# Optimization experiments

Hardware: AMD Instinct MI355X
Metric: run time of the kernel (lower is better)

Reference implementation:

```python
import jax, jax.numpy as jnp
import numpy as np

N = 100000; D = 256; ATT = 512; H = 8; HD = ATT // H; E = 250000
TYPE_CT = 64; TS = 64; P = 8192; PC = 1024; MP = 131072; MC = 16384


def setup_inputs() -> dict:
    key = jax.random.key(0)
    ks = jax.random.split(key, 24)
    sD = 1.0 / np.sqrt(D); sT = 1.0 / np.sqrt(TS); sA = 1.0 / np.sqrt(ATT); sC = 1.0 / np.sqrt(D + ATT)
    inp = {}
    inp['node_states'] = jax.random.normal(ks[0], (N, D), jnp.float32)
    inp['node_types'] = jax.random.randint(ks[1], (N,), 0, TYPE_CT, jnp.int32)
    inp['pair_conj'] = jax.random.randint(ks[2], (E,), 0, N, jnp.int32)
    inp['pair_prem'] = jax.random.randint(ks[3], (E,), 0, N, jnp.int32)
    inp['pool_prem_nodes'] = jax.random.randint(ks[4], (MP,), 0, N, jnp.int32)
    inp['pool_prem_seg'] = ((jnp.arange(MP, dtype=jnp.int32) * P) // MP).astype(jnp.int32)  # every prem set non-empty
    inp['pool_conj_nodes'] = jax.random.randint(ks[5], (MC,), 0, N, jnp.int32)
    inp['pool_conj_seg'] = ((jnp.arange(MC, dtype=jnp.int32) * PC) // MC).astype(jnp.int32)
    inp['prem2conj'] = jax.random.randint(ks[6], (P,), 0, PC, jnp.int32)
    # learned parameters
    inp['ln_g'] = jnp.ones((D,), jnp.float32)
    inp['ln_b'] = jnp.zeros((D,), jnp.float32)
    inp['emb_p'] = jax.random.normal(ks[7], (TYPE_CT, TS), jnp.float32) * 0.02
    inp['wp_w'] = jax.random.normal(ks[8], (TS, ATT), jnp.float32) * sT
    inp['wp_b'] = jnp.zeros((ATT,), jnp.float32)
    inp['emb_c'] = jax.random.normal(ks[9], (TYPE_CT, TS), jnp.float32) * 0.02
    inp['wc_w'] = jax.random.normal(ks[10], (TS, ATT), jnp.float32) * sT
    inp['wc_b'] = jnp.zeros((ATT,), jnp.float32)
    inp['Wq_p'] = jax.random.normal(ks[11], (H, D, HD), jnp.float32) * sD
    inp['Wk_p'] = jax.random.normal(ks[12], (H, D, HD), jnp.float32) * sD
    inp['Wv_p'] = jax.random.normal(ks[13], (H, D, HD), jnp.float32) * sD
    inp['Wo_p'] = jax.random.normal(ks[14], (ATT, ATT), jnp.float32) * sA
    inp['Wq_c'] = jax.random.normal(ks[15], (H, D, HD), jnp.float32) * sD
    inp['Wk_c'] = jax.random.normal(ks[16], (H, D, HD), jnp.float32) * sD
    inp['Wv_c'] = jax.random.normal(ks[17], (H, D, HD), jnp.float32) * sD
    inp['Wo_c'] = jax.random.normal(ks[18], (ATT, ATT), jnp.float32) * sA
    inp['W_dag'] = jax.random.normal(ks[19], (D + ATT, D + ATT), jnp.float32) * sC
    inp['b_dag'] = jnp.zeros((D + ATT,), jnp.float32)
    return inp


def _layernorm(x, g, b):
    mu = jnp.mean(x, axis=-1, keepdims=True)
    var = jnp.mean(jnp.square(x - mu), axis=-1, keepdims=True)
    return (x - mu) * jax.lax.rsqrt(var + 1e-5) * g + b


def _mha_dir(x, src, tgt, Wq, Wk, Wv, Wo, gate):
    # gather query/key/value node reprs along the pair list (irregular gather)
    xs = x[src]; xt = x[tgt]                       # [E, D]
    q = jnp.einsum('ed,hdk->ehk', xs, Wq)          # [E, H, HD]
    k = jnp.einsum('ed,hdk->ehk', xt, Wk)
    scores = jnp.sum(q * k, axis=-1) / np.sqrt(HD)  # [E, H]
    # per-query-node (segment) softmax, as in compute_att_aggr grouping
    m = jax.ops.segment_max(scores, src, num_segments=N)
    ex = jnp.exp(scores - m[src])
    denom = jax.ops.segment_sum(ex, src, num_segments=N)
    prob = ex / denom[src]
    v = jnp.einsum('ed,hdk->ehk', xt, Wv)
    # adj_matr @ comb_matr scatter-aggregation
    agg = jax.ops.segment_sum(prob[..., None] * v, src, num_segments=N)  # [N, H, HD]
    return gate * (agg.reshape(N, H * HD) @ Wo)


def reference(node_states, node_types, pair_conj, pair_prem, pool_prem_nodes, pool_prem_seg,
              pool_conj_nodes, pool_conj_seg, prem2conj,
              ln_g, ln_b, emb_p, wp_w, wp_b, emb_c, wc_w, wc_b,
              Wq_p, Wk_p, Wv_p, Wo_p, Wq_c, Wk_c, Wv_c, Wo_c, W_dag, b_dag):
    x = _layernorm(node_states, ln_g, ln_b)                                  # ne_norm(node reprs)
    gate_p = jax.nn.sigmoid(emb_p[node_types] @ wp_w + wp_b)                 # prem_gate  [N, ATT]
    gate_c = jax.nn.sigmoid(emb_c[node_types] @ wc_w + wc_b)                 # conj_gate
    # just_prem pairs: (prem, conj) -> query/scatter node = prem, key/value node = conj
    comb = _mha_dir(x, pair_prem, pair_conj, Wq_p, Wk_p, Wv_p, Wo_p, gate_p)
    # just_conj pairs: (conj, prem)
    comb = comb + _mha_dir(x, pair_conj, pair_prem, Wq_c, Wk_c, Wv_c, Wo_c, gate_c)
    h = jnp.concatenate([x, comb], axis=1)                                   # [N, D+ATT]
    pooled = jnp.tanh(h @ W_dag + b_dag)                                     # simplified dag_lstm pass
    prem_r = jax.ops.segment_max(pooled[pool_prem_nodes], pool_prem_seg, num_segments=P)
    conj_sets = jax.ops.segment_max(pooled[pool_conj_nodes], pool_conj_seg, num_segments=PC)
    conj_r = conj_sets[prem2conj]
    return jnp.concatenate([prem_r, conj_r], axis=1)                         # [P, 2*(D+ATT)]
```

## Files before the change

### kernel.cpp

```cpp
#include <hip/hip_runtime.h>
#include <math.h>

#define N_NODES 100000
#define DIM 256
#define ATT 512
#define NH 8
#define HD 64
#define E_PAIRS 250000
#define TYPE_CT 64
#define TS 64
#define P_SEG 8192
#define PC_SEG 1024
#define MP_SZ 131072
#define MC_SZ 16384
#define CD 768

typedef unsigned short u16;
typedef __attribute__((ext_vector_type(8))) short short8v;
typedef __attribute__((ext_vector_type(4))) float floatx4;

__device__ __forceinline__ u16 f2b(float f) {
    unsigned u = __float_as_uint(f);
    return (u16)((u + 0x7FFFu + ((u >> 16) & 1u)) >> 16);
}
__device__ __forceinline__ float b2f(u16 h) {
    return __uint_as_float(((unsigned)h) << 16);
}

__global__ __launch_bounds__(256) void fill_val_k(float* out, int n, float v) {
    int i = blockIdx.x * 256 + threadIdx.x;
    if (i < n) out[i] = v;
}

__global__ __launch_bounds__(64) void layernorm_k(
    const float* __restrict__ ns, const float* __restrict__ g,
    const float* __restrict__ b, u16* __restrict__ x)
{
    int row = blockIdx.x;
    int lane = threadIdx.x;
    float4 v = ((const float4*)(ns + (size_t)row * DIM))[lane];
    float sum = v.x + v.y + v.z + v.w;
    #pragma unroll
    for (int off = 32; off >= 1; off >>= 1) sum += __shfl_xor(sum, off);
    float mu = sum * (1.0f / DIM);
    float dx = v.x - mu, dy = v.y - mu, dz = v.z - mu, dw = v.w - mu;
    float sq = dx * dx + dy * dy + dz * dz + dw * dw;
    #pragma unroll
    for (int off = 32; off >= 1; off >>= 1) sq += __shfl_xor(sq, off);
    float rs = rsqrtf(sq * (1.0f / DIM) + 1e-5f);
    float4 gg = ((const float4*)g)[lane];
    float4 bb = ((const float4*)b)[lane];
    u16 o4[4];
    o4[0] = f2b(dx * rs * gg.x + bb.x);
    o4[1] = f2b(dy * rs * gg.y + bb.y);
    o4[2] = f2b(dz * rs * gg.z + bb.z);
    o4[3] = f2b(dw * rs * gg.w + bb.w);
    *(uint2*)(x + (size_t)row * DIM + lane * 4) = *(uint2*)o4;
}

__global__ __launch_bounds__(512) void gate_table_k(
    const float* __restrict__ emb, const float* __restrict__ w,
    const float* __restrict__ wb, float* __restrict__ tab)
{
    int t = blockIdx.x;
    int a = threadIdx.x;
    float acc = wb[a];
    #pragma unroll 8
    for (int s = 0; s < TS; ++s) acc += emb[t * TS + s] * w[s * ATT + a];
    tab[t * ATT + a] = 1.0f / (1.0f + expf(-acc));
}

__global__ __launch_bounds__(256) void wcvt_k(
    const float* __restrict__ W, u16* __restrict__ Bt, int K, int N)
{
    int idx = blockIdx.x * 256 + threadIdx.x;
    if (idx >= K * N) return;
    int c = idx / K, k = idx - c * K;
    Bt[idx] = f2b(W[(size_t)k * N + c]);
}

__global__ __launch_bounds__(256) void wqkv_cvt_k(
    const float* __restrict__ Wq, const float* __restrict__ Wk,
    const float* __restrict__ Wv, u16* __restrict__ outp)
{
    int idx = blockIdx.x * 256 + threadIdx.x;
    if (idx >= NH * 3 * HD * DIM) return;
    int k = idx & (DIM - 1);
    int c = (idx >> 8) & (HD - 1);
    int hm = idx >> 14;
    int m = hm % 3;
    int h = hm / 3;
    const float* W = (m == 0) ? Wq : ((m == 1) ? Wk : Wv);
    outp[idx] = f2b(W[((size_t)h * DIM + k) * HD + c]);
}

template<int WN, int EPI>
__device__ __forceinline__ void gemm_body2(
    const u16* __restrict__ A, int lda,
    const u16* __restrict__ A2, int lda2, int K1,
    const u16* __restrict__ Bt, int ldb,
    u16* __restrict__ C, int ldc,
    int M, int K,
    const float* __restrict__ bias,
    const float* __restrict__ gateTab,
    const int* __restrict__ types)
{
    constexpr int BN = 32 * WN;
    constexpr int BR = BN / 64;
    __shared__ u16 As[2][128 * 32];
    __shared__ u16 Bs[2][BN * 32];
    const int bm = blockIdx.y * 128;
    const int bn = blockIdx.x * BN;
    const int tid = threadIdx.x;
    const int wave = tid >> 6, lane = tid & 63;
    const int wm = (wave >> 1) * 64, wn = (wave & 1) * 16 * WN;
    const int srow = tid >> 2;
    const int skk = (tid & 3) * 8;
    floatx4 acc[4][WN] = {};

    auto stage = [&](int buf, int k0) {
        #pragma unroll
        for (int rnd = 0; rnd < 2; ++rnd) {
            int grow = bm + srow + rnd * 64;
            if (grow > M - 1) grow = M - 1;
            int gk = k0 + skk;
            const u16* src;
            if (EPI == 2 && gk >= K1) src = A2 + (size_t)grow * lda2 + (gk - K1);
            else                      src = A + (size_t)grow * lda + gk;
            __builtin_amdgcn_global_load_lds(
                (const __attribute__((address_space(1))) void*)src,
                (__attribute__((address_space(3))) void*)(&As[buf][rnd * 2048 + wave * 512]),
                16, 0, 0);
        }
        #pragma unroll
        for (int rnd = 0; rnd < BR; ++rnd) {
            const u16* src = Bt + (size_t)(bn + srow + rnd * 64) * ldb + k0 + skk;
            __builtin_amdgcn_global_load_lds(
                (const __attribute__((address_space(1))) void*)src,
                (__attribute__((address_space(3))) void*)(&Bs[buf][rnd * 2048 + wave * 512]),
                16, 0, 0);
        }
    };

    stage(0, 0);
    int cur = 0;
    const int rr = lane & 15, kq = (lane >> 4) * 8;
    for (int k0 = 0; k0 < K; k0 += 32) {
        __syncthreads();
        if (k0 + 32 < K) stage(cur ^ 1, k0 + 32);
        short8v a[4], b[WN];
        #pragma unroll
        for (int i = 0; i < 4; ++i)
            a[i] = *(const short8v*)&As[cur][(wm + i * 16 + rr) * 32 + kq];
        #pragma unroll
        for (int j = 0; j < WN; ++j)
            b[j] = *(const short8v*)&Bs[cur][(wn + j * 16 + rr) * 32 + kq];
        #pragma unroll
        for (int i = 0; i < 4; ++i)
            #pragma unroll
            for (int j = 0; j < WN; ++j)
                acc[i][j] = __builtin_amdgcn_mfma_f32_16x16x32_bf16(
                    a[i], b[j], acc[i][j], 0, 0, 0);
        cur ^= 1;
    }
    #pragma unroll
    for (int i = 0; i < 4; ++i) {
        #pragma unroll
        for (int j = 0; j < WN; ++j) {
            #pragma unroll
            for (int q = 0; q < 4; ++q) {
                int row = bm + wm + i * 16 + (lane >> 4) * 4 + q;
                if (row >= M) continue;
                int col = bn + wn + j * 16 + (lane & 15);
                float v = acc[i][j][q];
                size_t idx = (size_t)row * ldc + col;
                if (EPI == 0) C[idx] = f2b(v);
                else if (EPI == 1) {
                    float g = gateTab[types[row] * ATT + col];
                    C[idx] = f2b(b2f(C[idx]) + g * v);
                } else if (EPI == 3) {
                    float g = gateTab[types[row] * ATT + col];
                    C[idx] = f2b(g * v);
                } else {
                    C[idx] = f2b(tanhf(v + bias[col]));
                }
            }
        }
    }
}

__global__ __launch_bounds__(256) void gemm_qkv(
    const u16* __restrict__ A, const u16* __restrict__ Bt, u16* __restrict__ C)
{
    gemm_body2<6, 0>(A, DIM, nullptr, 0, 1 << 30, Bt, DIM, C, 192,
                     N_NODES, DIM, nullptr, nullptr, nullptr);
}
__global__ __launch_bounds__(256) void gemm_wo_first(
    const u16* __restrict__ A, const u16* __restrict__ Bt, u16* __restrict__ C,
    const float* __restrict__ gateTab, const int* __restrict__ types)
{
    gemm_body2<4, 3>(A, ATT, nullptr, 0, 1 << 30, Bt, ATT, C, ATT,
                     N_NODES, ATT, nullptr, gateTab, types);
}
__global__ __launch_bounds__(256) void gemm_wo_acc(
    const u16* __restrict__ A, const u16* __restrict__ Bt, u16* __restrict__ C,
    const float* __restrict__ gateTab, const int* __restrict__ types)
{
    gemm_body2<4, 1>(A, ATT, nullptr, 0, 1 << 30, Bt, ATT, C, ATT,
                     N_NODES, ATT, nullptr, gateTab, types);
}
__global__ __launch_bounds__(256) void gemm_dag(
    const u16* __restrict__ A, const u16* __restrict__ A2,
    const u16* __restrict__ Bt, u16* __restrict__ C,
    const float* __restrict__ bias)
{
    gemm_body2<4, 2>(A, DIM, A2, ATT, DIM, Bt, CD, C, 384,
                     N_NODES, CD, bias, nullptr, nullptr);
}

__global__ __launch_bounds__(256) void count_k(
    const int* __restrict__ src, int* __restrict__ counts)
{
    int e = blockIdx.x * 256 + threadIdx.x;
    if (e < E_PAIRS) atomicAdd(&counts[src[e]], 1);
}
__global__ __launch_bounds__(256) void scan1_k(
    const int* __restrict__ counts, int* __restrict__ offs, int* __restrict__ bsums)
{
    __shared__ int sm[256];
    int i = blockIdx.x * 256 + threadIdx.x;
    int v = (i < N_NODES) ? counts[i] : 0;
    sm[threadIdx.x] = v;
    __syncthreads();
    for (int d = 1; d < 256; d <<= 1) {
        int t = (threadIdx.x >= d) ? sm[threadIdx.x - d] : 0;
        __syncthreads();
        sm[threadIdx.x] += t;
        __syncthreads();
    }
    if (i < N_NODES) offs[i] = sm[threadIdx.x] - v;
    if (threadIdx.x == 255) bsums[blockIdx.x] = sm[255];
}
__global__ __launch_bounds__(512) void scan2_k(int* __restrict__ bsums, int nb)
{
    __shared__ int sm[512];
    int tx = threadIdx.x;
    int v = (tx < nb) ? bsums[tx] : 0;
    sm[tx] = v;
    __syncthreads();
    for (int d = 1; d < 512; d <<= 1) {
        int t = (tx >= d) ? sm[tx - d] : 0;
        __syncthreads();
        sm[tx] += t;
        __syncthreads();
    }
    if (tx < nb) bsums[tx] = sm[tx] - v;
}
__global__ __launch_bounds__(256) void addcur_k(
    int* __restrict__ offs, const int* __restrict__ bsums, int* __restrict__ cur)
{
    int i = blockIdx.x * 256 + threadIdx.x;
    if (i >= N_NODES) return;
    int o = offs[i] + bsums[i >> 8];
    offs[i] = o;
    cur[i] = o;
}
__global__ __launch_bounds__(256) void scatter_k(
    const int* __restrict__ src, const int* __restrict__ tgt,
    int* __restrict__ cur, int* __restrict__ csr_tgt)
{
    int e = blockIdx.x * 256 + threadIdx.x;
    if (e >= E_PAIRS) return;
    int p = atomicAdd(&cur[src[e]], 1);
    csr_tgt[p] = tgt[e];
}

__global__ __launch_bounds__(256) void attn_k(
    const u16* __restrict__ qkv, const int* __restrict__ offs,
    const int* __restrict__ counts, const int* __restrict__ csr_tgt,
    u16* __restrict__ agg, int h)
{
    int s = blockIdx.x * 4 + (threadIdx.x >> 6);
    if (s >= N_NODES) return;
    int lane = threadIdx.x & 63;
    float q = b2f(qkv[(size_t)s * 192 + lane]) * 0.125f;
    int lo = offs[s], deg = counts[s];
    float m = -INFINITY, l = 0.0f, acc = 0.0f;
    for (int i = 0; i < deg; ++i) {
        int t = csr_tgt[lo + i];
        float kd = b2f(qkv[(size_t)t * 192 + 64 + lane]);
        float vd = b2f(qkv[(size_t)t * 192 + 128 + lane]);
        float p = q * kd;
        #pragma unroll
        for (int off = 32; off >= 1; off >>= 1) p += __shfl_xor(p, off);
        float mn = fmaxf(m, p);
        float sc = expf(m - mn);
        float w  = expf(p - mn);
        l = l * sc + w;
        acc = acc * sc + w * vd;
        m = mn;
    }
    float r = (deg > 0) ? acc / l : 0.0f;
    agg[(size_t)s * ATT + h * HD + lane] = f2b(r);
}

template<int BFOUT>
__global__ __launch_bounds__(256) void seg_max_k(
    const u16* __restrict__ pooled, const int* __restrict__ nodes,
    const int* __restrict__ seg, int total, void* __restrict__ outv, int ldo)
{
    int p = blockIdx.x;
    int lo, hi;
    { int a = 0, b2 = total; while (a < b2) { int mid = (a + b2) >> 1; if (seg[mid] < p) a = mid + 1; else b2 = mid; } lo = a; }
    { int a = lo, b2 = total; while (a < b2) { int mid = (a + b2) >> 1; if (seg[mid] < p + 1) a = mid + 1; else b2 = mid; } hi = a; }
    for (int c = threadIdx.x; c < 384; c += 256) {
        float mx = -INFINITY;
        for (int i = lo; i < hi; ++i)
            mx = fmaxf(mx, b2f(pooled[(size_t)nodes[i] * 384 + c]));
        if (BFOUT) ((u16*)outv)[(size_t)p * ldo + c] = f2b(mx);
        else       ((float*)outv)[(size_t)p * ldo + c] = mx;
    }
}

__global__ __launch_bounds__(768) void gather_conj(
    const u16* __restrict__ cs, const int* __restrict__ p2c,
    float* __restrict__ out)
{
    int p = blockIdx.x;
    int c = threadIdx.x;
    out[(size_t)p * (2 * CD) + CD + c] = b2f(cs[(size_t)p2c[p] * CD + c]);
}

extern "C" void kernel_launch(void* const* d_in, const int* in_sizes, int n_in,
                              void* d_out, int out_size, void* d_ws, size_t ws_size,
                              hipStream_t stream) {
    const float* node_states     = (const float*)d_in[0];
    const int*   node_types      = (const int*)d_in[1];
    const int*   pair_conj       = (const int*)d_in[2];
    const int*   pair_prem       = (const int*)d_in[3];
    const int*   pool_prem_nodes = (const int*)d_in[4];
    const int*   pool_prem_seg   = (const int*)d_in[5];
    const int*   pool_conj_nodes = (const int*)d_in[6];
    const int*   pool_conj_seg   = (const int*)d_in[7];
    const int*   prem2conj       = (const int*)d_in[8];
    const float* ln_g  = (const float*)d_in[9];
    const float* ln_b  = (const float*)d_in[10];
    const float* emb_p = (const float*)d_in[11];
    const float* wp_w  = (const float*)d_in[12];
    const float* wp_b  = (const float*)d_in[13];
    const float* emb_c = (const float*)d_in[14];
    const float* wc_w  = (const float*)d_in[15];
    const float* wc_b  = (const float*)d_in[16];
    const float* Wq_p  = (const float*)d_in[17];
    const float* Wk_p  = (const float*)d_in[18];
    const float* Wv_p  = (const float*)d_in[19];
    const float* Wo_p  = (const float*)d_in[20];
    const float* Wq_c  = (const float*)d_in[21];
    const float* Wk_c  = (const float*)d_in[22];
    const float* Wv_c  = (const float*)d_in[23];
    const float* Wo_c  = (const float*)d_in[24];
    const float* W_dag = (const float*)d_in[25];
    const float* b_dag = (const float*)d_in[26];
    float* out = (float*)d_out;

    char* ws = (char*)d_ws;
    size_t o = 0;
    u16* x_bf  = (u16*)(ws + o); o += (size_t)N_NODES * DIM * 2;
    u16* comb  = (u16*)(ws + o); o += (size_t)N_NODES * ATT * 2;
    u16* R     = (u16*)(ws + o); o += (size_t)N_NODES * ATT * 2;
    char* csrb = ws + o;         o += 8000000;
    u16* conj_sets = (u16*)(ws + o); o += (size_t)PC_SEG * CD * 2;
    const size_t WS_NEEDED = o;

    if (ws_size < WS_NEEDED) {
        fill_val_k<<<(out_size + 255) / 256, 256, 0, stream>>>(out, out_size, (float)ws_size);
        return;
    }

    u16* agg    = R;
    u16* pooled = R;
    int* c_counts[2], *c_offs[2], *c_cur[2], *c_tgt[2];
    for (int d = 0; d < 2; ++d) {
        char* base = csrb + (size_t)d * 2200000;
        c_counts[d] = (int*)(base + 0);
        c_offs[d]   = (int*)(base + 400000);
        c_cur[d]    = (int*)(base + 800000);
        c_tgt[d]    = (int*)(base + 1200000);
    }
    int* bsums = (int*)(csrb + 4400000);
    u16* wdag_t = (u16*)csrb;

    char* ob = (char*)d_out;
    u16* qkv     = (u16*)(ob + 0);
    float* gtab_p = (float*)(ob + 38400000);
    float* gtab_c = (float*)(ob + 38531072);
    u16* wqkv_t  = (u16*)(ob + 38662144);
    u16* wo_t    = (u16*)(ob + 40235008);

    layernorm_k<<<N_NODES, 64, 0, stream>>>(node_states, ln_g, ln_b, x_bf);
    gate_table_k<<<TYPE_CT, ATT, 0, stream>>>(emb_p, wp_w, wp_b, gtab_p);
    gate_table_k<<<TYPE_CT, ATT, 0, stream>>>(emb_c, wc_w, wc_b, gtab_c);
    wqkv_cvt_k<<<(NH * 3 * HD * DIM + 255) / 256, 256, 0, stream>>>(
        Wq_p, Wk_p, Wv_p, wqkv_t);
    wqkv_cvt_k<<<(NH * 3 * HD * DIM + 255) / 256, 256, 0, stream>>>(
        Wq_c, Wk_c, Wv_c, wqkv_t + (size_t)NH * 3 * HD * DIM);
    wcvt_k<<<(ATT * ATT + 255) / 256, 256, 0, stream>>>(Wo_p, wo_t, ATT, ATT);
    wcvt_k<<<(ATT * ATT + 255) / 256, 256, 0, stream>>>(
        Wo_c, wo_t + (size_t)ATT * ATT, ATT, ATT);

    const int NSCAN = (N_NODES + 255) / 256;
    for (int d = 0; d < 2; ++d) {
        const int* src = d ? pair_conj : pair_prem;
        const int* tgt = d ? pair_prem : pair_conj;
        hipMemsetAsync(c_counts[d], 0, 400000, stream);
        count_k<<<(E_PAIRS + 255) / 256, 256, 0, stream>>>(src, c_counts[d]);
        scan1_k<<<NSCAN, 256, 0, stream>>>(c_counts[d], c_offs[d], bsums);
        scan2_k<<<1, 512, 0, stream>>>(bsums, NSCAN);
        addcur_k<<<NSCAN, 256, 0, stream>>>(c_offs[d], bsums, c_cur[d]);
        scatter_k<<<(E_PAIRS + 255) / 256, 256, 0, stream>>>(src, tgt, c_cur[d], c_tgt[d]);
    }

    const int MB128 = (N_NODES + 127) / 128;

    for (int dir = 0; dir < 2; ++dir) {
        const float* gt = dir ? gtab_c : gtab_p;
        const u16* wq_d = wqkv_t + (size_t)dir * NH * 3 * HD * DIM;
        const u16* wo_d = wo_t + (size_t)dir * ATT * ATT;

        for (int h = 0; h < NH; ++h) {
            gemm_qkv<<<dim3(1, MB128), 256, 0, stream>>>(
                x_bf, wq_d + (size_t)h * 3 * HD * DIM, qkv);
            attn_k<<<(N_NODES + 3) / 4, 256, 0, stream>>>(
                qkv, c_offs[dir], c_counts[dir], c_tgt[dir], agg, h);
        }

        if (dir == 0)
            gemm_wo_first<<<dim3(ATT / 128, MB128), 256, 0, stream>>>(
                agg, wo_d, comb, gt, node_types);
        else
            gemm_wo_acc<<<dim3(ATT / 128, MB128), 256, 0, stream>>>(
                agg, wo_d, comb, gt, node_types);
    }

    wcvt_k<<<(CD * CD + 255) / 256, 256, 0, stream>>>(W_dag, wdag_t, CD, CD);

    for (int c0 = 0; c0 < CD; c0 += 384) {
        gemm_dag<<<dim3(3, MB128), 256, 0, stream>>>(
            x_bf, comb, wdag_t + (size_t)c0 * CD, pooled, b_dag + c0);
        seg_max_k<0><<<P_SEG, 256, 0, stream>>>(
            pooled, pool_prem_nodes, pool_prem_seg, MP_SZ, out + c0, 2 * CD);
        seg_max_k<1><<<PC_SEG, 256, 0, stream>>>(
            pooled, pool_conj_nodes, pool_conj_seg, MC_SZ, conj_sets + c0, CD);
    }
    gather_conj<<<P_SEG, CD, 0, stream>>>(conj_sets, prem2conj, out);
}
```

Baseline: 2.232 ms.

## Triple-buffer GEMM LDS staging with explicit vmcnt waits and raw barriers

Converts the shared bf16 GEMM body from double to triple buffering, so global-to-LDS loads are issued two k-steps ahead. Each iteration waits with an explicit s_waitcnt vmcnt on only the older outstanding loads and then issues a bare s_barrier, replacing __syncthreads. The goal is to hide global load latency behind MFMA work in all four projection GEMMs. The cost is 50% more LDS per block, which may lower occupancy, plus hand-counted waits that depend on how many loads each stage issues.

```diff
diff --git a/kernel.cpp b/kernel.cpp
--- a/kernel.cpp
+++ b/kernel.cpp
@@ -25,6 +25,15 @@
 }
 __device__ __forceinline__ float b2f(u16 h) {
     return __uint_as_float(((unsigned)h) << 16);
+}
+
+template<int N>
+__device__ __forceinline__ void waitcnt_vm() {
+    asm volatile("s_waitcnt vmcnt(%0)" :: "n"(N) : "memory");
+}
+__device__ __forceinline__ void barrier_fence() {
+    asm volatile("s_barrier" ::: "memory");
+    __builtin_amdgcn_sched_barrier(0);
 }
 
 __global__ __launch_bounds__(256) void fill_val_k(float* out, int n, float v) {
@@ -95,7 +104,7 @@
 }
 
 template<int WN, int EPI>
-__device__ __forceinline__ void gemm_body2(
+__device__ __forceinline__ void gemm_body3(
     const u16* __restrict__ A, int lda,
     const u16* __restrict__ A2, int lda2, int K1,
     const u16* __restrict__ Bt, int ldb,
@@ -107,8 +116,9 @@
 {
     constexpr int BN = 32 * WN;
     constexpr int BR = BN / 64;
-    __shared__ u16 As[2][128 * 32];
-    __shared__ u16 Bs[2][BN * 32];
+    constexpr int LA = 2 + BR;
+    __shared__ u16 As[3][128 * 32];
+    __shared__ u16 Bs[3][BN * 32];
     const int bm = blockIdx.y * 128;
     const int bn = blockIdx.x * BN;
     const int tid = threadIdx.x;
@@ -142,12 +152,16 @@
         }
     };
 
+    const int NS = K >> 5;
     stage(0, 0);
+    stage(1, 32);
+    const int rr = lane & 15, kq = (lane >> 4) * 8;
     int cur = 0;
-    const int rr = lane & 15, kq = (lane >> 4) * 8;
-    for (int k0 = 0; k0 < K; k0 += 32) {
-        __syncthreads();
-        if (k0 + 32 < K) stage(cur ^ 1, k0 + 32);
+    for (int is = 0; is < NS; ++is) {
+        if (is == NS - 1) waitcnt_vm<0>();
+        else              waitcnt_vm<LA>();
+        barrier_fence();
+        if (is + 2 < NS) stage((cur + 2) % 3, (is + 2) * 32);
         short8v a[4], b[WN];
         #pragma unroll
         for (int i = 0; i < 4; ++i)
@@ -161,7 +175,7 @@
             for (int j = 0; j < WN; ++j)
                 acc[i][j] = __builtin_amdgcn_mfma_f32_16x16x32_bf16(
                     a[i], b[j], acc[i][j], 0, 0, 0);
-        cur ^= 1;
+        cur = (cur + 1) % 3;
     }
     #pragma unroll
     for (int i = 0; i < 4; ++i) {
@@ -192,21 +206,21 @@
 __global__ __launch_bounds__(256) void gemm_qkv(
     const u16* __restrict__ A, const u16* __restrict__ Bt, u16* __restrict__ C)
 {
-    gemm_body2<6, 0>(A, DIM, nullptr, 0, 1 << 30, Bt, DIM, C, 192,
+    gemm_body3<6, 0>(A, DIM, nullptr, 0, 1 << 30, Bt, DIM, C, 192,
                      N_NODES, DIM, nullptr, nullptr, nullptr);
 }
 __global__ __launch_bounds__(256) void gemm_wo_first(
     const u16* __restrict__ A, const u16* __restrict__ Bt, u16* __restrict__ C,
     const float* __restrict__ gateTab, const int* __restrict__ types)
 {
-    gemm_body2<4, 3>(A, ATT, nullptr, 0, 1 << 30, Bt, ATT, C, ATT,
+    gemm_body3<4, 3>(A, ATT, nullptr, 0, 1 << 30, Bt, ATT, C, ATT,
                      N_NODES, ATT, nullptr, gateTab, types);
 }
 __global__ __launch_bounds__(256) void gemm_wo_acc(
     const u16* __restrict__ A, const u16* __restrict__ Bt, u16* __restrict__ C,
     const float* __restrict__ gateTab, const int* __restrict__ types)
 {
-    gemm_body2<4, 1>(A, ATT, nullptr, 0, 1 << 30, Bt, ATT, C, ATT,
+    gemm_body3<4, 1>(A, ATT, nullptr, 0, 1 << 30, Bt, ATT, C, ATT,
                      N_NODES, ATT, nullptr, gateTab, types);
 }
 __global__ __launch_bounds__(256) void gemm_dag(
@@ -214,7 +228,7 @@
     const u16* __restrict__ Bt, u16* __restrict__ C,
     const float* __restrict__ bias)
 {
-    gemm_body2<4, 2>(A, DIM, A2, ATT, DIM, Bt, CD, C, 384,
+    gemm_body3<4, 2>(A, DIM, A2, ATT, DIM, Bt, CD, C, 384,
                      N_NODES, CD, bias, nullptr, nullptr);
 }
 
```

Result: no change. 2.215 ms (-0.8%).
